# Performance work log

Measured on AMD Instinct MI355X. Metric: run time of the kernel, lower is better.

The kernel has to match this reference:

```python
import jax, jax.numpy as jnp
import numpy as np

B, T, CIN, H, W = 1, 8, 32, 256, 256
CO, NH, WS = 64, 8, 8  # C_out, n_head, wind_size


def conv3x3(x, w, b):
    # x: [N, C, h, w], w: [O, I, 3, 3], stride 1, padding 1 (SAME for 3x3)
    y = jax.lax.conv_general_dilated(
        x, w, window_strides=(1, 1), padding=((1, 1), (1, 1)),
        dimension_numbers=("NCHW", "OIHW", "NCHW"))
    return y + b[None, :, None, None]


def setup_inputs() -> dict:
    key = jax.random.key(0)
    ks = jax.random.split(key, 9)
    s = 0.05  # small init scale keeps attention logits well-conditioned
    f32 = jnp.float32
    return {
        "x": jax.random.normal(ks[0], (B, T, CIN, H, W), f32),
        "Wq": jax.random.normal(ks[1], (CO, CIN, 3, 3), f32) * s,
        "bq": jax.random.normal(ks[2], (CO,), f32) * s,
        "Wk": jax.random.normal(ks[3], (CO, CIN, 3, 3), f32) * s,
        "bk": jax.random.normal(ks[4], (CO,), f32) * s,
        "Wv": jax.random.normal(ks[5], (CO, CIN, 3, 3), f32) * s,
        "bv": jax.random.normal(ks[6], (CO,), f32) * s,
        "Wo": jax.random.normal(ks[7], (CO, CO, 3, 3), f32) * s,
        "bo": jax.random.normal(ks[8], (CO,), f32) * s,
    }


def reference(x, Wq, bq, Wk, bk, Wv, bv, Wo, bo):
    b, t, c, h, w = x.shape
    Hg, Wg = h // WS, w // WS          # grid of windows
    hc = CO // NH                      # per-head channels
    d = hc * WS * WS                   # per-window token dim

    # im2grid: [B,T,C,H,W] -> [B*T*Hg*Wg, C, Ws, Ws] (each window a conv batch elem)
    xg = (x.reshape(b, t, c, Hg, WS, Wg, WS)
           .transpose(0, 1, 3, 5, 2, 4, 6)
           .reshape(b * t * Hg * Wg, c, WS, WS))

    def proj(wgt, bias):
        y = conv3x3(xg, wgt, bias)                        # [BTHWg, CO, Ws, Ws]
        y = y.reshape(b, t, Hg * Wg, NH, hc, WS, WS)      # split heads (nh outer in channel)
        return y.transpose(0, 1, 3, 2, 4, 5, 6).reshape(b, t, NH, Hg * Wg, d)

    q, k, v = proj(Wq, bq), proj(Wk, bk), proj(Wv, bv)    # [B,T,nh,HWg,d]

    att = jnp.einsum("btnqd,btnkd->btnqk", q, k) * (1.0 / np.sqrt(d)).astype(x.dtype)
    att = jax.nn.softmax(att, axis=-1)                    # [B,T,nh,HWg,HWg]
    y = jnp.einsum("btnqk,btnkd->btnqd", att, v)          # [B,T,nh,HWg,d]

    # back to image: [B,T,nh,HWg,hc,Ws,Ws] -> [B,T,CO,Hg,Wg,Ws,Ws] -> [B,T,CO,H,W]
    y = (y.reshape(b, t, NH, Hg * Wg, hc, WS, WS)
          .transpose(0, 1, 2, 4, 3, 5, 6)
          .reshape(b, t, CO, Hg, Wg, WS, WS)
          .transpose(0, 1, 2, 3, 5, 4, 6)
          .reshape(b, t, CO, h, w))

    out = y + conv3x3(y.reshape(b * t, CO, h, w), Wo, bo).reshape(b, t, CO, h, w)
    return out
```

## Files before the change

### kernel.cpp

```cpp
#include <hip/hip_runtime.h>
#include <hip/hip_bf16.h>
#include <stdint.h>


using bf16 = __hip_bfloat16;
typedef short bf16x8 __attribute__((ext_vector_type(8)));
typedef float f32x4 __attribute__((ext_vector_type(4)));

#define AS1 __attribute__((address_space(1)))
#define AS3 __attribute__((address_space(3)))

__device__ __forceinline__ void gload_lds16(const void* g, void* l) {
  __builtin_amdgcn_global_load_lds((const AS1 unsigned int*)g, (AS3 unsigned int*)l, 16, 0, 0);
}
__device__ __forceinline__ float b2f(unsigned short u) {
  union { unsigned int i; float f; } x; x.i = ((unsigned)u) << 16; return x.f;
}
__device__ __forceinline__ unsigned short f2b(float f) {
  __hip_bfloat16 h = __float2bfloat16(f);
  return *reinterpret_cast<unsigned short*>(&h);
}

__global__ __launch_bounds__(256) void prep_w(const float* __restrict__ Wq, const float* __restrict__ Wk,
                                              const float* __restrict__ Wv, const float* __restrict__ Wo,
                                              bf16* __restrict__ wt, bf16* __restrict__ wot) {
  int i = blockIdx.x * 256 + threadIdx.x;
  if (i < 9 * 192 * 32) {
    int ci = i & 31, co192 = (i >> 5) % 192, s = i / 6144;
    int dy = s / 3, dx = s % 3;
    int proj = co192 >> 6, co = co192 & 63;
    const float* Ws = (proj == 0) ? Wq : ((proj == 1) ? Wk : Wv);
    wt[i] = __float2bfloat16(Ws[((co * 32 + ci) * 3 + dy) * 3 + dx]);
  }
  if (i < 9 * 64 * 64) {
    int ci = i & 63, co = (i >> 6) & 63, s = i >> 12;
    wot[i] = __float2bfloat16(Wo[((co * 64 + ci) * 3 + (s / 3)) * 3 + (s % 3)]);
  }
}

__global__ __launch_bounds__(256) void qkv_conv(const float* __restrict__ x, const bf16* __restrict__ wt,
                                                const float* __restrict__ bq, const float* __restrict__ bk,
                                                const float* __restrict__ bv,
                                                bf16* __restrict__ qout, bf16* __restrict__ kout,
                                                bf16* __restrict__ vout) {
  __shared__ bf16 smem[192 * 136];
  bf16* xp = smem;
  int tid = threadIdx.x, bid = blockIdx.x;
  int t = bid >> 9, g = bid & 511;
  int gy = g >> 4, gx0 = (g & 15) * 2;

  unsigned int* xp32 = (unsigned int*)xp;
  for (int i = tid; i < 4000; i += 256) xp32[i] = 0u;
  __syncthreads();
  const float* xb = x + (size_t)t * 32 * 65536;
  #pragma unroll
  for (int it = 0; it < 16; ++it) {
    int e = tid + it * 256;
    int ix = e & 7, win = (e >> 3) & 1, iy = (e >> 4) & 7, ci = e >> 7;
    float val = xb[(size_t)ci * 65536 + (gy * 8 + iy) * 256 + (gx0 + win) * 8 + ix];
    xp[(win * 100 + (iy + 1) * 10 + (ix + 1)) * 40 + ci] = __float2bfloat16(val);
  }
  __syncthreads();

  int wv = tid >> 6, l = tid & 63, l15 = l & 15, lg = l >> 4;
  f32x4 z4 = {0.f, 0.f, 0.f, 0.f};
  f32x4 acc[3][8];
  for (int i = 0; i < 3; ++i) for (int j = 0; j < 8; ++j) acc[i][j] = z4;

  #pragma unroll
  for (int s = 0; s < 9; ++s) {
    const int dy = s / 3, dx = s % 3;
    bf16x8 a[3];
    #pragma unroll
    for (int mt = 0; mt < 3; ++mt)
      a[mt] = *(const bf16x8*)&wt[((size_t)s * 192 + wv * 48 + mt * 16 + l15) * 32 + lg * 8];
    #pragma unroll
    for (int nt = 0; nt < 8; ++nt) {
      int n = nt * 16 + l15;
      int win = n >> 6, px = n & 63;
      int iy = px >> 3, ix = px & 7;
      bf16x8 b = *(const bf16x8*)&xp[(win * 100 + (iy + dy) * 10 + (ix + dx)) * 40 + lg * 8];
      #pragma unroll
      for (int mt = 0; mt < 3; ++mt)
        acc[mt][nt] = __builtin_amdgcn_mfma_f32_16x16x32_bf16(a[mt], b, acc[mt][nt], 0, 0, 0);
    }
  }

  __syncthreads();
  bf16* outl = smem;
  #pragma unroll
  for (int mt = 0; mt < 3; ++mt) {
    int c0 = wv * 48 + mt * 16 + lg * 4;
    int proj = c0 >> 6;
    const float* bptr = (proj == 0) ? bq : ((proj == 1) ? bk : bv);
    float bias[4];
    #pragma unroll
    for (int r = 0; r < 4; ++r) bias[r] = bptr[(c0 + r) & 63];
    #pragma unroll
    for (int nt = 0; nt < 8; ++nt) {
      int n = nt * 16 + l15;
      #pragma unroll
      for (int r = 0; r < 4; ++r)
        outl[(c0 + r) * 136 + n] = __float2bfloat16(acc[mt][nt][r] + bias[r]);
    }
  }
  __syncthreads();

  #pragma unroll
  for (int proj = 0; proj < 3; ++proj) {
    bf16* dst = (proj == 0) ? qout : ((proj == 1) ? kout : vout);
    #pragma unroll
    for (int pass = 0; pass < 4; ++pass) {
      int c = pass * 256 + tid;
      int d8 = c & 63, head = (c >> 6) & 7, wn2 = c >> 9;
      int jj = d8 >> 3, px0 = (d8 & 7) * 8;
      bf16x8 val = *(const bf16x8*)&outl[(proj * 64 + head * 8 + jj) * 136 + wn2 * 64 + px0];
      size_t gwin = (size_t)gy * 32 + gx0 + wn2;
      *(bf16x8*)&dst[((size_t)(t * 8 + head) * 1024 + gwin) * 512 + d8 * 8] = val;
    }
  }
}

__global__ __launch_bounds__(256) void transpose_v(const bf16* __restrict__ v, bf16* __restrict__ vt) {
  __shared__ bf16 tl[64 * 72];
  int tid = threadIdx.x, bid = blockIdx.x;
  int bh = bid >> 7, wtile = (bid >> 3) & 15, dtile = bid & 7;
  int w0 = wtile * 64, d0 = dtile * 64;
  const bf16* vb = v + ((size_t)bh * 1024 + w0) * 512 + d0;
  int win_l = tid >> 2, dseg = (tid & 3) * 16;
  bf16x8 x0 = *(const bf16x8*)&vb[(size_t)win_l * 512 + dseg];
  bf16x8 x1 = *(const bf16x8*)&vb[(size_t)win_l * 512 + dseg + 8];
  #pragma unroll
  for (int j = 0; j < 8; ++j) {
    *(short*)&tl[(dseg + j) * 72 + win_l] = x0[j];
    *(short*)&tl[(dseg + 8 + j) * 72 + win_l] = x1[j];
  }
  __syncthreads();
  int d_l = tid >> 2, wseg = (tid & 3) * 16;
  bf16x8 y0 = *(const bf16x8*)&tl[d_l * 72 + wseg];
  bf16x8 y1 = *(const bf16x8*)&tl[d_l * 72 + wseg + 8];
  bf16* vtb = vt + ((size_t)bh * 512 + d_l * 8 + dtile) * 1024 + w0 + wseg;
  *(bf16x8*)&vtb[0] = y0;
  *(bf16x8*)&vtb[8] = y1;
}

__device__ __forceinline__ void stage8(const bf16* __restrict__ Ab, const bf16* __restrict__ Bb,
                                       bf16* smem, int c, int t, int sk,
                                       int w, int lr, int sl) {
  #pragma unroll
  for (int p = 0; p < 4; ++p) {
    int row = p * 64 + w * 8 + lr;
    gload_lds16(Ab + (size_t)row * sk + t * 64 + sl * 8,
                (char*)smem + c * 65536 + p * 8192 + w * 1024);
    gload_lds16(Bb + (size_t)row * sk + t * 64 + sl * 8,
                (char*)smem + c * 65536 + 32768 + p * 8192 + w * 1024);
  }
}

__global__ __launch_bounds__(512, 2) void qk_gemm(const bf16* __restrict__ q, const bf16* __restrict__ k,
                                                  bf16* __restrict__ S) {
  __shared__ bf16 smem[65536];
  int tid = threadIdx.x;
  int bid = (blockIdx.x & 7) * 128 + (blockIdx.x >> 3);
  int batch = bid >> 4, tm = (bid >> 2) & 3, tn = bid & 3;
  const bf16* Qb = q + (size_t)batch * 1024 * 512 + (size_t)tm * 256 * 512;
  const bf16* Kb = k + (size_t)batch * 1024 * 512 + (size_t)tn * 256 * 512;
  int w = tid >> 6, l = tid & 63, l15 = l & 15, lg = l >> 4;
  int wm2 = w >> 2, wn4 = w & 3;
  int lr = l >> 3, sl = (l & 7) ^ lr, swz = l15 & 7;
  f32x4 z4 = {0.f, 0.f, 0.f, 0.f};
  f32x4 acc[8][4];
  for (int i = 0; i < 8; ++i) for (int j = 0; j < 4; ++j) acc[i][j] = z4;

  stage8(Qb, Kb, smem, 0, 0, 512, w, lr, sl);
  asm volatile("s_waitcnt vmcnt(0)" ::: "memory");
  __builtin_amdgcn_s_barrier();
  __builtin_amdgcn_sched_barrier(0);

  for (int t = 0; t < 8; ++t) {
    int c = t & 1;
    if (t + 1 < 8) stage8(Qb, Kb, smem, c ^ 1, t + 1, 512, w, lr, sl);
    const bf16* At = smem + c * 32768;
    const bf16* Bt = At + 16384;
    __builtin_amdgcn_s_setprio(1);
    #pragma unroll
    for (int kk = 0; kk < 2; ++kk) {
      int ps = (kk * 4 + lg) ^ swz;
      bf16x8 a[8], b[4];
      #pragma unroll
      for (int i = 0; i < 8; ++i)
        a[i] = *(const bf16x8*)&At[(wm2 * 128 + i * 16 + l15) * 64 + ps * 8];
      #pragma unroll
      for (int j = 0; j < 4; ++j)
        b[j] = *(const bf16x8*)&Bt[(wn4 * 64 + j * 16 + l15) * 64 + ps * 8];
      #pragma unroll
      for (int i = 0; i < 8; ++i)
        #pragma unroll
        for (int j = 0; j < 4; ++j)
          acc[i][j] = __builtin_amdgcn_mfma_f32_16x16x32_bf16(a[i], b[j], acc[i][j], 0, 0, 0);
    }
    __builtin_amdgcn_s_setprio(0);
    asm volatile("s_waitcnt vmcnt(0)" ::: "memory");
    __builtin_amdgcn_s_barrier();
    __builtin_amdgcn_sched_barrier(0);
  }

  const float SCALE = 0.04419417382415922f;
  bf16* Sb = S + (size_t)batch * 1024 * 1024;
  #pragma unroll
  for (int i = 0; i < 8; ++i)
    #pragma unroll
    for (int j = 0; j < 4; ++j)
      #pragma unroll
      for (int r = 0; r < 4; ++r) {
        int row = tm * 256 + wm2 * 128 + i * 16 + lg * 4 + r;
        int col = tn * 256 + wn4 * 64 + j * 16 + l15;
        Sb[(size_t)row * 1024 + col] = __float2bfloat16(acc[i][j][r] * SCALE);
      }
}

__global__ __launch_bounds__(256) void softmax_rows(bf16* __restrict__ S) {
  int l = threadIdx.x & 63;
  size_t row = (size_t)blockIdx.x * 4 + (threadIdx.x >> 6);
  bf16* p = S + row * 1024 + l * 16;
  bf16x8 s0 = *(const bf16x8*)p;
  bf16x8 s1 = *(const bf16x8*)(p + 8);
  float f[16];
  #pragma unroll
  for (int i = 0; i < 8; ++i) { f[i] = b2f((unsigned short)s0[i]); f[8 + i] = b2f((unsigned short)s1[i]); }
  float m = f[0];
  #pragma unroll
  for (int i = 1; i < 16; ++i) m = fmaxf(m, f[i]);
  for (int d = 1; d < 64; d <<= 1) m = fmaxf(m, __shfl_xor(m, d));
  float sum = 0.f;
  #pragma unroll
  for (int i = 0; i < 16; ++i) { f[i] = __expf(f[i] - m); sum += f[i]; }
  for (int d = 1; d < 64; d <<= 1) sum += __shfl_xor(sum, d);
  float r = 1.0f / sum;
  bf16x8 o0, o1;
  #pragma unroll
  for (int i = 0; i < 8; ++i) { o0[i] = (short)f2b(f[i] * r); o1[i] = (short)f2b(f[8 + i] * r); }
  *(bf16x8*)p = o0;
  *(bf16x8*)(p + 8) = o1;
}

__global__ __launch_bounds__(512, 2) void pv_gemm(const bf16* __restrict__ P, const bf16* __restrict__ vt,
                                                  bf16* __restrict__ y) {
  __shared__ bf16 smem[65536];
  int tid = threadIdx.x;
  int bid = (blockIdx.x & 7) * 64 + (blockIdx.x >> 3);
  int batch = bid >> 3, bq = (bid >> 1) & 3, bd = bid & 1;
  const bf16* Pb = P + (size_t)batch * 1024 * 1024 + (size_t)bq * 256 * 1024;
  const bf16* Vb = vt + (size_t)batch * 512 * 1024 + (size_t)bd * 256 * 1024;
  int w = tid >> 6, l = tid & 63, l15 = l & 15, lg = l >> 4;
  int wm2 = w >> 2, wn4 = w & 3;
  int lr = l >> 3, sl = (l & 7) ^ lr, swz = l15 & 7;
  f32x4 z4 = {0.f, 0.f, 0.f, 0.f};
  f32x4 acc[8][4];
  for (int i = 0; i < 8; ++i) for (int j = 0; j < 4; ++j) acc[i][j] = z4;

  stage8(Pb, Vb, smem, 0, 0, 1024, w, lr, sl);
  asm volatile("s_waitcnt vmcnt(0)" ::: "memory");
  __builtin_amdgcn_s_barrier();
  __builtin_amdgcn_sched_barrier(0);

  for (int t = 0; t < 16; ++t) {
    int c = t & 1;
    if (t + 1 < 16) stage8(Pb, Vb, smem, c ^ 1, t + 1, 1024, w, lr, sl);
    const bf16* At = smem + c * 32768;
    const bf16* Bt = At + 16384;
    __builtin_amdgcn_s_setprio(1);
    #pragma unroll
    for (int kk = 0; kk < 2; ++kk) {
      int ps = (kk * 4 + lg) ^ swz;
      bf16x8 a[8], b[4];
      #pragma unroll
      for (int i = 0; i < 8; ++i)
        a[i] = *(const bf16x8*)&At[(wm2 * 128 + i * 16 + l15) * 64 + ps * 8];
      #pragma unroll
      for (int j = 0; j < 4; ++j)
        b[j] = *(const bf16x8*)&Bt[(wn4 * 64 + j * 16 + l15) * 64 + ps * 8];
      #pragma unroll
      for (int i = 0; i < 8; ++i)
        #pragma unroll
        for (int j = 0; j < 4; ++j)
          acc[i][j] = __builtin_amdgcn_mfma_f32_16x16x32_bf16(a[i], b[j], acc[i][j], 0, 0, 0);
    }
    __builtin_amdgcn_s_setprio(0);
    asm volatile("s_waitcnt vmcnt(0)" ::: "memory");
    __builtin_amdgcn_s_barrier();
    __builtin_amdgcn_sched_barrier(0);
  }

  int t2 = batch >> 3, h = batch & 7;
  #pragma unroll
  for (int i = 0; i < 8; ++i)
    #pragma unroll
    for (int j = 0; j < 4; ++j)
      #pragma unroll
      for (int r = 0; r < 4; ++r) {
        int win = bq * 256 + wm2 * 128 + i * 16 + lg * 4 + r;
        int dp = bd * 256 + wn4 * 64 + j * 16 + l15;
        int jj = dp & 7, pyix = dp >> 3;
        int gy = win >> 5, gx = win & 31;
        int Y = gy * 8 + (pyix >> 3), X = gx * 8 + (pyix & 7);
        y[(((size_t)t2 * 256 + Y) * 256 + X) * 64 + h * 8 + jj] = __float2bfloat16(acc[i][j][r]);
      }
}

__global__ __launch_bounds__(256) void out_conv(const bf16* __restrict__ yimg, const bf16* __restrict__ wot,
                                                const float* __restrict__ bo, float* __restrict__ out) {
  __shared__ bf16 yp[324 * 76];
  int tid = threadIdx.x, bid = blockIdx.x;
  int t = bid >> 8, tile = bid & 255;
  int y0 = (tile >> 4) * 16, x0 = (tile & 15) * 16;
  const bf16* yb = yimg + (size_t)t * 256 * 256 * 64;

  for (int e = tid; e < 324 * 8; e += 256) {
    int seg = e & 7, pos = e >> 3;
    int ppx = pos % 18, ppy = pos / 18;
    int gy = y0 + ppy - 1, gx = x0 + ppx - 1;
    bf16x8 val = {0, 0, 0, 0, 0, 0, 0, 0};
    if ((unsigned)gy < 256u && (unsigned)gx < 256u)
      val = *(const bf16x8*)&yb[((size_t)gy * 256 + gx) * 64 + seg * 8];
    *(bf16x8*)&yp[pos * 76 + seg * 8] = val;
  }
  __syncthreads();

  int wv = tid >> 6, l = tid & 63, l15 = l & 15, lg = l >> 4;
  int wm = wv & 1, wn = wv >> 1;
  f32x4 z4 = {0.f, 0.f, 0.f, 0.f};
  f32x4 acc[2][8];
  for (int i = 0; i < 2; ++i) for (int j = 0; j < 8; ++j) acc[i][j] = z4;

  #pragma unroll
  for (int s9 = 0; s9 < 9; ++s9) {
    const int dy = s9 / 3, dx = s9 % 3;
    #pragma unroll
    for (int half = 0; half < 2; ++half) {
      bf16x8 a[2];
      #pragma unroll
      for (int mt = 0; mt < 2; ++mt)
        a[mt] = *(const bf16x8*)&wot[((size_t)s9 * 64 + wm * 32 + mt * 16 + l15) * 64 + half * 32 + lg * 8];
      #pragma unroll
      for (int nt = 0; nt < 8; ++nt) {
        int ty = wn * 8 + nt;
        bf16x8 b = *(const bf16x8*)&yp[((ty + dy) * 18 + l15 + dx) * 76 + half * 32 + lg * 8];
        #pragma unroll
        for (int mt = 0; mt < 2; ++mt)
          acc[mt][nt] = __builtin_amdgcn_mfma_f32_16x16x32_bf16(a[mt], b, acc[mt][nt], 0, 0, 0);
      }
    }
  }

  float* ob = out + (size_t)t * 64 * 65536;
  float bias[2][4];
  #pragma unroll
  for (int mt = 0; mt < 2; ++mt)
    #pragma unroll
    for (int r = 0; r < 4; ++r) bias[mt][r] = bo[wm * 32 + mt * 16 + lg * 4 + r];
  #pragma unroll
  for (int mt = 0; mt < 2; ++mt)
    #pragma unroll
    for (int nt = 0; nt < 8; ++nt) {
      int ty = wn * 8 + nt;
      #pragma unroll
      for (int r = 0; r < 4; ++r) {
        int co = wm * 32 + mt * 16 + lg * 4 + r;
        float res = b2f(*(const unsigned short*)&yp[((ty + 1) * 18 + l15 + 1) * 76 + co]);
        ob[(size_t)co * 65536 + (size_t)(y0 + ty) * 256 + x0 + l15] = res + acc[mt][nt][r] + bias[mt][r];
      }
    }
}

extern "C" void kernel_launch(void* const* d_in, const int* in_sizes, int n_in,
                              void* d_out, int out_size, void* d_ws, size_t ws_size,
                              hipStream_t stream) {
  const float* x  = (const float*)d_in[0];
  const float* Wq = (const float*)d_in[1];
  const float* bq = (const float*)d_in[2];
  const float* Wk = (const float*)d_in[3];
  const float* bk = (const float*)d_in[4];
  const float* Wv = (const float*)d_in[5];
  const float* bv = (const float*)d_in[6];
  const float* Wo = (const float*)d_in[7];
  const float* bo = (const float*)d_in[8];
  float* out = (float*)d_out;

  char* ws = (char*)d_ws;
  bf16* wt  = (bf16*)(ws + 0);
  bf16* wot = (bf16*)(ws + 110592);
  bf16* q   = (bf16*)(ws + 262144);
  bf16* k   = (bf16*)(ws + 67371008);
  bf16* v   = (bf16*)(ws + 134479872);
  bf16* S   = (bf16*)(ws + 134479872);
  bf16* vt  = (bf16*)(ws + 268697600);
  bf16* y   = (bf16*)(ws + 262144);

  prep_w<<<216, 256, 0, stream>>>(Wq, Wk, Wv, Wo, wt, wot);
  qkv_conv<<<4096, 256, 0, stream>>>(x, wt, bq, bk, bv, q, k, v);
  transpose_v<<<8192, 256, 0, stream>>>(v, vt);
  qk_gemm<<<1024, 512, 0, stream>>>(q, k, S);
  softmax_rows<<<16384, 256, 0, stream>>>(S);
  pv_gemm<<<512, 512, 0, stream>>>(S, vt, y);
  out_conv<<<2048, 256, 0, stream>>>(y, wot, bo, out);
}
```

Before: 451.5 us.

## Shrink qkv_conv LDS footprint and vectorize channel-major input staging

Cuts the qkv_conv shared buffer from 192x136 to 64x136 bf16 elements. The epilogue now stages and writes out one projection at a time, with extra barriers between them. Only the halo border of the padded input tile is zeroed, not the whole tile. Each thread loads 16 channels for one pixel and writes them to LDS as two 16-byte vector stores instead of scalar bf16 stores. The aim is higher occupancy and fewer LDS write instructions, at the cost of serialized epilogue phases and more syncs.

```diff
diff --git a/kernel.cpp b/kernel.cpp
--- a/kernel.cpp
+++ b/kernel.cpp
@@ -43,22 +43,39 @@
                                                 const float* __restrict__ bv,
                                                 bf16* __restrict__ qout, bf16* __restrict__ kout,
                                                 bf16* __restrict__ vout) {
-  __shared__ bf16 smem[192 * 136];
+  __shared__ bf16 smem[8704];
   bf16* xp = smem;
   int tid = threadIdx.x, bid = blockIdx.x;
   int t = bid >> 9, g = bid & 511;
   int gy = g >> 4, gx0 = (g & 15) * 2;
 
   unsigned int* xp32 = (unsigned int*)xp;
-  for (int i = tid; i < 4000; i += 256) xp32[i] = 0u;
-  __syncthreads();
-  const float* xb = x + (size_t)t * 32 * 65536;
-  #pragma unroll
-  for (int it = 0; it < 16; ++it) {
-    int e = tid + it * 256;
-    int ix = e & 7, win = (e >> 3) & 1, iy = (e >> 4) & 7, ci = e >> 7;
-    float val = xb[(size_t)ci * 65536 + (gy * 8 + iy) * 256 + (gx0 + win) * 8 + ix];
-    xp[(win * 100 + (iy + 1) * 10 + (ix + 1)) * 40 + ci] = __float2bfloat16(val);
+  for (int i = tid; i < 1440; i += 256) {
+    int win = i / 720, rem = i - win * 720;
+    int h = rem / 20, dwi = rem - h * 20;
+    int py, px;
+    if (h < 10)      { py = 0; px = h; }
+    else if (h < 20) { py = 9; px = h - 10; }
+    else if (h < 28) { py = h - 19; px = 0; }
+    else             { py = h - 27; px = 9; }
+    xp32[(win * 100 + py * 10 + px) * 20 + dwi] = 0u;
+  }
+
+  {
+    int s4 = tid & 127;
+    int winS = s4 >> 6, pyS = (s4 >> 3) & 7, pxS = s4 & 7;
+    int ci0 = (tid >> 7) * 16;
+    const float* xs = x + (size_t)t * 32 * 65536 + (size_t)(gy * 8 + pyS) * 256 + (gx0 + winS) * 8 + pxS;
+    short vv[16];
+    #pragma unroll
+    for (int c = 0; c < 16; ++c)
+      vv[c] = (short)f2b(xs[(size_t)(ci0 + c) * 65536]);
+    bf16x8 w0, w1;
+    #pragma unroll
+    for (int j = 0; j < 8; ++j) { w0[j] = vv[j]; w1[j] = vv[8 + j]; }
+    bf16* dstl = &xp[(winS * 100 + (pyS + 1) * 10 + (pxS + 1)) * 40 + ci0];
+    *(bf16x8*)dstl = w0;
+    *(bf16x8*)(dstl + 8) = w1;
   }
   __syncthreads();
 
@@ -89,35 +106,34 @@
   __syncthreads();
   bf16* outl = smem;
   #pragma unroll
-  for (int mt = 0; mt < 3; ++mt) {
-    int c0 = wv * 48 + mt * 16 + lg * 4;
-    int proj = c0 >> 6;
-    const float* bptr = (proj == 0) ? bq : ((proj == 1) ? bk : bv);
-    float bias[4];
-    #pragma unroll
-    for (int r = 0; r < 4; ++r) bias[r] = bptr[(c0 + r) & 63];
-    #pragma unroll
-    for (int nt = 0; nt < 8; ++nt) {
-      int n = nt * 16 + l15;
-      #pragma unroll
-      for (int r = 0; r < 4; ++r)
-        outl[(c0 + r) * 136 + n] = __float2bfloat16(acc[mt][nt][r] + bias[r]);
-    }
-  }
-  __syncthreads();
-
-  #pragma unroll
-  for (int proj = 0; proj < 3; ++proj) {
-    bf16* dst = (proj == 0) ? qout : ((proj == 1) ? kout : vout);
-    #pragma unroll
-    for (int pass = 0; pass < 4; ++pass) {
-      int c = pass * 256 + tid;
-      int d8 = c & 63, head = (c >> 6) & 7, wn2 = c >> 9;
-      int jj = d8 >> 3, px0 = (d8 & 7) * 8;
-      bf16x8 val = *(const bf16x8*)&outl[(proj * 64 + head * 8 + jj) * 136 + wn2 * 64 + px0];
-      size_t gwin = (size_t)gy * 32 + gx0 + wn2;
+  for (int p = 0; p < 3; ++p) {
+    const float* bptr = (p == 0) ? bq : ((p == 1) ? bk : bv);
+    bf16* dst = (p == 0) ? qout : ((p == 1) ? kout : vout);
+    #pragma unroll
+    for (int mt = 0; mt < 3; ++mt) {
+      int c0 = wv * 48 + mt * 16;
+      if ((c0 >> 6) != p) continue;
+      float bias[4];
+      #pragma unroll
+      for (int r = 0; r < 4; ++r) bias[r] = bptr[(c0 + lg * 4 + r) & 63];
+      #pragma unroll
+      for (int nt = 0; nt < 8; ++nt) {
+        int n = nt * 16 + l15;
+        #pragma unroll
+        for (int r = 0; r < 4; ++r)
+          outl[((c0 + lg * 4 + r) & 63) * 136 + n] = __float2bfloat16(acc[mt][nt][r] + bias[r]);
+      }
+    }
+    __syncthreads();
+    #pragma unroll
+    for (int it = 0; it < 4; ++it) {
+      int c = it * 256 + tid;
+      int d8 = c & 63, head = (c >> 6) & 7, win2 = c >> 9;
+      bf16x8 val = *(const bf16x8*)&outl[(head * 8 + (d8 >> 3)) * 136 + win2 * 64 + (d8 & 7) * 8];
+      size_t gwin = (size_t)gy * 32 + gx0 + win2;
       *(bf16x8*)&dst[((size_t)(t * 8 + head) * 1024 + gwin) * 512 + d8 * 8] = val;
     }
+    if (p < 2) __syncthreads();
   }
 }
 
```

Result: slower. 512.7 us (+13.6%).

## Fuse softmax normalization into PV GEMM A-tile staging using precomputed row stats

Applied to the files above, without the earlier changes.

Softmax is split in two. A row_stats kernel only reads S and writes a per-row max and reciprocal sum, and pv_gemm loads raw score tiles into registers, applies exp and normalization, and writes the result to LDS. This removes the full 128 MB bf16 write-back of the probability matrix. In exchange it adds exp math and a register round-trip in the GEMM's staging path, which can reduce overlap with the MFMA loop. Each pair of GEMM tiles over the same rows recomputes the exponentials.

```diff
diff --git a/kernel.cpp b/kernel.cpp
--- a/kernel.cpp
+++ b/kernel.cpp
@@ -219,10 +219,10 @@
       }
 }
 
-__global__ __launch_bounds__(256) void softmax_rows(bf16* __restrict__ S) {
+__global__ __launch_bounds__(256) void row_stats(const bf16* __restrict__ S, float2* __restrict__ pstats) {
   int l = threadIdx.x & 63;
   size_t row = (size_t)blockIdx.x * 4 + (threadIdx.x >> 6);
-  bf16* p = S + row * 1024 + l * 16;
+  const bf16* p = S + row * 1024 + l * 16;
   bf16x8 s0 = *(const bf16x8*)p;
   bf16x8 s1 = *(const bf16x8*)(p + 8);
   float f[16];
@@ -234,23 +234,22 @@
   for (int d = 1; d < 64; d <<= 1) m = fmaxf(m, __shfl_xor(m, d));
   float sum = 0.f;
   #pragma unroll
-  for (int i = 0; i < 16; ++i) { f[i] = __expf(f[i] - m); sum += f[i]; }
+  for (int i = 0; i < 16; ++i) sum += __expf(f[i] - m);
   for (int d = 1; d < 64; d <<= 1) sum += __shfl_xor(sum, d);
-  float r = 1.0f / sum;
-  bf16x8 o0, o1;
-  #pragma unroll
-  for (int i = 0; i < 8; ++i) { o0[i] = (short)f2b(f[i] * r); o1[i] = (short)f2b(f[8 + i] * r); }
-  *(bf16x8*)p = o0;
-  *(bf16x8*)(p + 8) = o1;
-}
-
-__global__ __launch_bounds__(512, 2) void pv_gemm(const bf16* __restrict__ P, const bf16* __restrict__ vt,
+  if (l == 0) {
+    float2 st; st.x = m; st.y = 1.0f / sum;
+    pstats[row] = st;
+  }
+}
+
+__global__ __launch_bounds__(512, 2) void pv_gemm(const bf16* __restrict__ S, const bf16* __restrict__ vt,
+                                                  const float2* __restrict__ pstats,
                                                   bf16* __restrict__ y) {
   __shared__ bf16 smem[65536];
   int tid = threadIdx.x;
   int bid = (blockIdx.x & 7) * 64 + (blockIdx.x >> 3);
   int batch = bid >> 3, bq = (bid >> 1) & 3, bd = bid & 1;
-  const bf16* Pb = P + (size_t)batch * 1024 * 1024 + (size_t)bq * 256 * 1024;
+  const bf16* Pb = S + (size_t)batch * 1024 * 1024 + (size_t)bq * 256 * 1024;
   const bf16* Vb = vt + (size_t)batch * 512 * 1024 + (size_t)bd * 256 * 1024;
   int w = tid >> 6, l = tid & 63, l15 = l & 15, lg = l >> 4;
   int wm2 = w >> 2, wn4 = w & 3;
@@ -259,14 +258,49 @@
   f32x4 acc[8][4];
   for (int i = 0; i < 8; ++i) for (int j = 0; j < 4; ++j) acc[i][j] = z4;
 
-  stage8(Pb, Vb, smem, 0, 0, 1024, w, lr, sl);
+  float m4[4], r4[4];
+  #pragma unroll
+  for (int p = 0; p < 4; ++p) {
+    float2 st = pstats[(size_t)batch * 1024 + bq * 256 + p * 64 + w * 8 + lr];
+    m4[p] = st.x; r4[p] = st.y;
+  }
+
+  bf16x8 areg[4];
+  #define PV_ISSUE(tt, cc)                                                        \
+    {                                                                             \
+      _Pragma("unroll")                                                           \
+      for (int p = 0; p < 4; ++p)                                                 \
+        areg[p] = *(const bf16x8*)&Pb[(size_t)(p * 64 + w * 8 + lr) * 1024 +      \
+                                      (tt) * 64 + sl * 8];                        \
+      _Pragma("unroll")                                                           \
+      for (int p = 0; p < 4; ++p)                                                 \
+        gload_lds16(Vb + (size_t)(p * 64 + w * 8 + lr) * 1024 + (tt) * 64 + sl * 8, \
+                    (char*)smem + (cc) * 65536 + 32768 + p * 8192 + w * 1024);    \
+    }
+  #define PV_WRITE_A(cc)                                                          \
+    {                                                                             \
+      _Pragma("unroll")                                                           \
+      for (int p = 0; p < 4; ++p) {                                               \
+        bf16x8 o;                                                                 \
+        _Pragma("unroll")                                                         \
+        for (int e = 0; e < 8; ++e) {                                             \
+          float fv = b2f((unsigned short)areg[p][e]);                             \
+          o[e] = (short)f2b(__expf(fv - m4[p]) * r4[p]);                          \
+        }                                                                         \
+        *(bf16x8*)((char*)smem + (cc) * 65536 + p * 8192 + w * 1024 + l * 16) = o; \
+      }                                                                           \
+    }
+
+  PV_ISSUE(0, 0);
   asm volatile("s_waitcnt vmcnt(0)" ::: "memory");
+  PV_WRITE_A(0);
+  asm volatile("s_waitcnt lgkmcnt(0)" ::: "memory");
   __builtin_amdgcn_s_barrier();
   __builtin_amdgcn_sched_barrier(0);
 
   for (int t = 0; t < 16; ++t) {
     int c = t & 1;
-    if (t + 1 < 16) stage8(Pb, Vb, smem, c ^ 1, t + 1, 1024, w, lr, sl);
+    if (t + 1 < 16) PV_ISSUE(t + 1, c ^ 1);
     const bf16* At = smem + c * 32768;
     const bf16* Bt = At + 16384;
     __builtin_amdgcn_s_setprio(1);
@@ -288,6 +322,8 @@
     }
     __builtin_amdgcn_s_setprio(0);
     asm volatile("s_waitcnt vmcnt(0)" ::: "memory");
+    if (t + 1 < 16) PV_WRITE_A(c ^ 1);
+    asm volatile("s_waitcnt lgkmcnt(0)" ::: "memory");
     __builtin_amdgcn_s_barrier();
     __builtin_amdgcn_sched_barrier(0);
   }
@@ -392,6 +428,7 @@
   bf16* wot = (bf16*)(ws + 110592);
   bf16* q   = (bf16*)(ws + 262144);
   bf16* k   = (bf16*)(ws + 67371008);
+  float2* pstats = (float2*)(ws + 67371008);
   bf16* v   = (bf16*)(ws + 134479872);
   bf16* S   = (bf16*)(ws + 134479872);
   bf16* vt  = (bf16*)(ws + 268697600);
@@ -401,7 +438,7 @@
   qkv_conv<<<4096, 256, 0, stream>>>(x, wt, bq, bk, bv, q, k, v);
   transpose_v<<<8192, 256, 0, stream>>>(v, vt);
   qk_gemm<<<1024, 512, 0, stream>>>(q, k, S);
-  softmax_rows<<<16384, 256, 0, stream>>>(S);
-  pv_gemm<<<512, 512, 0, stream>>>(S, vt, y);
+  row_stats<<<16384, 256, 0, stream>>>(S, pstats);
+  pv_gemm<<<512, 512, 0, stream>>>(S, vt, pstats, y);
   out_conv<<<2048, 256, 0, stream>>>(y, wot, bo, out);
 }
```

After: 442.1 us. -2.1%, faster.
